# Kernel optimization log

Measured on AMD Instinct MI355X. Metric: run time of the kernel, lower is better.

Reference implementation:

```python
import jax, jax.numpy as jnp
import numpy as np

OUT_F, IN_F = 4096, 11008
NUMEL = OUT_F * IN_F            # divisible by 256
NUM_SUPER = NUMEL // 256        # super-blocks of 8 sub-blocks x 32 values


def setup_inputs() -> dict:
    key = jax.random.key(0)
    k = jax.random.split(key, 7)
    x = jax.random.normal(k[0], (64, IN_F), dtype=jnp.float32)
    packed = jax.random.randint(k[1], (NUMEL // 2,), 0, 256, dtype=jnp.int32)
    d = jax.random.uniform(k[2], (NUM_SUPER,), dtype=jnp.float32) * 0.02
    dmin = jax.random.uniform(k[3], (NUM_SUPER,), dtype=jnp.float32) * 0.02
    scales = jax.random.randint(k[4], (NUM_SUPER * 8,), 0, 64, dtype=jnp.int32)
    mins = jax.random.randint(k[5], (NUM_SUPER * 8,), 0, 64, dtype=jnp.int32)
    bias = jax.random.normal(k[6], (OUT_F,), dtype=jnp.float32) * 0.02
    return {"x": x, "packed": packed, "d": d, "dmin": dmin,
            "scales": scales, "mins": mins, "bias": bias}


def _dequant_q4k(packed, d, dmin, scales, mins):
    # unpack two 4-bit quants per byte, interleaved low/high (stack dim=1 + flatten)
    low = packed & 15
    high = (packed >> 4) & 15
    q = jnp.stack([low, high], axis=1).reshape(NUM_SUPER, 8, 32).astype(jnp.float32)
    sc = (scales.astype(jnp.float32) / 63.0).reshape(NUM_SUPER, 8, 1)
    mn = (mins.astype(jnp.float32) / 63.0).reshape(NUM_SUPER, 8, 1)
    normalized = q / 15.0 * sc + mn
    w = normalized * d.reshape(NUM_SUPER, 1, 1) + dmin.reshape(NUM_SUPER, 1, 1)
    return w.reshape(OUT_F, IN_F)


def reference(x, packed, d, dmin, scales, mins, bias):
    w = _dequant_q4k(packed, d, dmin, scales, mins)   # [OUT_F, IN_F] fp32
    return x @ w.T + bias                              # F.linear
```

## Files before the change

kernel.cpp:

```cpp
#include <hip/hip_runtime.h>
#include <stdint.h>

#define OUT_F   4096
#define IN_F    11008
#define BATCH   64
#define NSUP    43
#define SB_ROW  344
#define IPR     5504
#define NKS     12
#define XP_BYTES   (4 * 344 * 64 * 16)
#define PART_ELEMS ((size_t)NKS * BATCH * OUT_F)
#define WS_FULL    (XP_BYTES + PART_ELEMS * 4)

typedef __attribute__((ext_vector_type(8))) short  short8;
typedef __attribute__((ext_vector_type(4))) float  floatx4;
typedef __attribute__((ext_vector_type(4))) int    intx4;

__device__ __forceinline__ unsigned pack_bf16(float f0, float f1) {
    return __builtin_amdgcn_perm(__float_as_uint(f1), __float_as_uint(f0), 0x07060302u);
}

__global__ __launch_bounds__(256) void xprep_kernel(const float* __restrict__ x,
                                                    intx4* __restrict__ xp) {
    const int ksb = blockIdx.x;
    const int mt  = threadIdx.x >> 6;
    const int l   = threadIdx.x & 63;
    const int lo  = l & 15, hi = l >> 4;
    const float* src = x + (mt * 16 + lo) * IN_F + ksb * 32 + hi * 8;
    floatx4 a0 = *(const floatx4*)src;
    floatx4 a1 = *(const floatx4*)(src + 4);
    intx4 r;
    r.x = pack_bf16(a0.x, a0.y);
    r.y = pack_bf16(a0.z, a0.w);
    r.z = pack_bf16(a1.x, a1.y);
    r.w = pack_bf16(a1.z, a1.w);
    xp[(mt * 344 + ksb) * 64 + l] = r;
}

__global__ __launch_bounds__(256) void init_out_kernel(const float* __restrict__ bias,
                                                       float* __restrict__ out) {
    int i = blockIdx.x * 256 + threadIdx.x;
    out[i] = bias[i & (OUT_F - 1)];
}

__global__ __launch_bounds__(256) void reduce_kernel(const float* __restrict__ part,
                                                     const float* __restrict__ bias,
                                                     float* __restrict__ out) {
    const int i = blockIdx.x * 256 + threadIdx.x;
    float s = bias[i & (OUT_F - 1)];
    #pragma unroll
    for (int k = 0; k < NKS; ++k) s += part[(size_t)k * (BATCH * OUT_F) + i];
    out[i] = s;
}

template<bool USE_PART>
__global__ __launch_bounds__(256, 3) void qlin_main(
    const intx4* __restrict__ xp,
    const int*   __restrict__ packed,
    const float* __restrict__ dd,
    const float* __restrict__ dmn_g,
    const int*   __restrict__ scales,
    const int*   __restrict__ mins,
    float*       __restrict__ part,
    float*       __restrict__ out)
{
    __shared__ intx4 xfs[2048];
    __shared__ int   scs[512];
    __shared__ int   mns[512];
    __shared__ float dsx[64];
    __shared__ float dmx[64];

    const int nb  = blockIdx.x & 63;
    const int ks  = blockIdx.x >> 6;
    const int tid = threadIdx.x;
    const int w   = tid >> 6;
    const int l   = tid & 63;
    const int lo  = l & 15, hi = l >> 4;

    const int o    = nb * 64 + w * 16 + lo;
    const int r    = w * 16 + lo;
    const int sup0 = ks < 7 ? 4 * ks : 28 + 3 * (ks - 7);
    const int nsup = ks < 7 ? 4 : 3;

    floatx4 acc[4];
    #pragma unroll
    for (int mt = 0; mt < 4; ++mt) acc[mt] = (floatx4)0.0f;

    const int* bp0 = packed + o * IPR + sup0 * 128 + hi * 4;
    const int tr = tid & 63;
    const int og = nb * 64 + tr;

    #pragma unroll 1
    for (int s = 0; s < nsup; ++s) {
        const int sup = sup0 + s;

        intx4 br[8];
        #pragma unroll
        for (int st = 0; st < 8; ++st)
            br[st] = __builtin_nontemporal_load((const intx4*)(bp0 + s * 128 + st * 16));

        intx4 xtmp[8];
        const intx4* xsrc = xp + sup * 512;
        #pragma unroll
        for (int i = 0; i < 8; ++i) {
            const int idx = i * 256 + tid;
            xtmp[i] = xsrc[(idx >> 9) * 22016 + (idx & 511)];
        }
        intx4 sct0, sct1;
        float dtmp = 0.0f;
        if (w == 0) {
            sct0 = *(const intx4*)(scales + og * SB_ROW + sup * 8);
            sct1 = *(const intx4*)(scales + og * SB_ROW + sup * 8 + 4);
        } else if (w == 1) {
            sct0 = *(const intx4*)(mins + og * SB_ROW + sup * 8);
            sct1 = *(const intx4*)(mins + og * SB_ROW + sup * 8 + 4);
        } else if (w == 2) {
            dtmp = dd[og * NSUP + sup];
        } else {
            dtmp = dmn_g[og * NSUP + sup];
        }

        if (s > 0) __syncthreads();
        #pragma unroll
        for (int i = 0; i < 8; ++i)
            xfs[i * 256 + tid] = xtmp[i];
        if (w == 0) {
            *(intx4*)&scs[tr * 8]     = sct0;
            *(intx4*)&scs[tr * 8 + 4] = sct1;
        } else if (w == 1) {
            *(intx4*)&mns[tr * 8]     = sct0;
            *(intx4*)&mns[tr * 8 + 4] = sct1;
        } else if (w == 2) {
            dsx[tr] = dtmp;
        } else {
            dmx[tr] = dtmp;
        }
        __syncthreads();

        const float dv   = dsx[r];
        const float dmv  = dmx[r];
        const float A945 = dv * (1.0f / 945.0f);
        const float A63  = dv * (1.0f / 63.0f);
        const intx4 s0 = *(const intx4*)&scs[r * 8];
        const intx4 s1 = *(const intx4*)&scs[r * 8 + 4];
        const intx4 m0 = *(const intx4*)&mns[r * 8];
        const intx4 m1 = *(const intx4*)&mns[r * 8 + 4];

        #pragma unroll
        for (int st = 0; st < 8; ++st) {
            const int scv = (st < 4) ? s0[st & 3] : s1[st & 3];
            const int mnv = (st < 4) ? m0[st & 3] : m1[st & 3];
            const float A = A945 * (float)scv;
            const float B = fmaf(A63, (float)mnv, dmv);
            const int v0 = br[st].x, v1 = br[st].y, v2 = br[st].z, v3 = br[st].w;
            union { intx4 i; short8 s8; } uw;
            uw.i.x = pack_bf16(fmaf((float)(v0 & 15), A, B), fmaf((float)(v0 >> 4), A, B));
            uw.i.y = pack_bf16(fmaf((float)(v1 & 15), A, B), fmaf((float)(v1 >> 4), A, B));
            uw.i.z = pack_bf16(fmaf((float)(v2 & 15), A, B), fmaf((float)(v2 >> 4), A, B));
            uw.i.w = pack_bf16(fmaf((float)(v3 & 15), A, B), fmaf((float)(v3 >> 4), A, B));

            union { intx4 i; short8 s8; } u0, u1, u2, u3;
            u0.i = xfs[0 * 512 + st * 64 + l];
            u1.i = xfs[1 * 512 + st * 64 + l];
            u2.i = xfs[2 * 512 + st * 64 + l];
            u3.i = xfs[3 * 512 + st * 64 + l];
            acc[0] = __builtin_amdgcn_mfma_f32_16x16x32_bf16(u0.s8, uw.s8, acc[0], 0, 0, 0);
            acc[1] = __builtin_amdgcn_mfma_f32_16x16x32_bf16(u1.s8, uw.s8, acc[1], 0, 0, 0);
            acc[2] = __builtin_amdgcn_mfma_f32_16x16x32_bf16(u2.s8, uw.s8, acc[2], 0, 0, 0);
            acc[3] = __builtin_amdgcn_mfma_f32_16x16x32_bf16(u3.s8, uw.s8, acc[3], 0, 0, 0);
        }
    }

    if (USE_PART) {
        float* pbase = part + (size_t)ks * (BATCH * OUT_F) + o;
        #pragma unroll
        for (int mt = 0; mt < 4; ++mt) {
            #pragma unroll
            for (int rr = 0; rr < 4; ++rr)
                pbase[(mt * 16 + hi * 4 + rr) * OUT_F] = acc[mt][rr];
        }
    } else {
        #pragma unroll
        for (int mt = 0; mt < 4; ++mt) {
            #pragma unroll
            for (int rr = 0; rr < 4; ++rr)
                atomicAdd(out + (mt * 16 + hi * 4 + rr) * OUT_F + o, acc[mt][rr]);
        }
    }
}

extern "C" void kernel_launch(void* const* d_in, const int* in_sizes, int n_in,
                              void* d_out, int out_size, void* d_ws, size_t ws_size,
                              hipStream_t stream) {
    (void)in_sizes; (void)n_in; (void)out_size;
    const float* x      = (const float*)d_in[0];
    const int*   packed = (const int*)d_in[1];
    const float* d      = (const float*)d_in[2];
    const float* dmin   = (const float*)d_in[3];
    const int*   scales = (const int*)d_in[4];
    const int*   mins   = (const int*)d_in[5];
    const float* bias   = (const float*)d_in[6];
    float* out = (float*)d_out;

    const bool has_part = ws_size >= (size_t)WS_FULL;
    intx4* xp   = (intx4*)d_ws;
    float* part = (float*)((char*)d_ws + XP_BYTES);

    xprep_kernel<<<344, 256, 0, stream>>>(x, xp);

    if (has_part) {
        qlin_main<true><<<64 * NKS, 256, 0, stream>>>(
            xp, packed, d, dmin, scales, mins, part, out);
        reduce_kernel<<<(BATCH * OUT_F) / 256, 256, 0, stream>>>(part, bias, out);
    } else {
        init_out_kernel<<<(BATCH * OUT_F) / 256, 256, 0, stream>>>(bias, out);
        qlin_main<false><<<64 * NKS, 256, 0, stream>>>(
            xp, packed, d, dmin, scales, mins, part, out);
    }
}
```

Measured before the change: 166.3 us.

## Prefetch next weight block in registers and stage x via direct global-to-LDS loads

Restructures the main loop into a software pipeline. The next super-block's packed weights and scale metadata are loaded into registers while the current one is computed. Activation tiles are copied straight from global memory into LDS with global_load_lds instead of round-tripping through VGPRs. Each thread now loads its own row's scales, mins and d values directly, which removes the shared-memory staging for them. The cost is higher register pressure from double-buffered weights under a launch bound of 3 waves, plus a full vmcnt(0) wait that also drains the prefetch loads before each barrier.

```diff
diff --git a/kernel.cpp b/kernel.cpp
--- a/kernel.cpp
+++ b/kernel.cpp
@@ -16,8 +16,22 @@
 typedef __attribute__((ext_vector_type(4))) float  floatx4;
 typedef __attribute__((ext_vector_type(4))) int    intx4;
 
+template<int N> struct IC { static constexpr int value = N; };
+
 __device__ __forceinline__ unsigned pack_bf16(float f0, float f1) {
     return __builtin_amdgcn_perm(__float_as_uint(f1), __float_as_uint(f0), 0x07060302u);
+}
+
+__device__ __forceinline__ void glds16(const void* g, void* s) {
+    __builtin_amdgcn_global_load_lds(
+        (const __attribute__((address_space(1))) uint32_t*)g,
+        (__attribute__((address_space(3))) uint32_t*)s,
+        16, 0, 0);
+}
+
+__device__ __forceinline__ void wait_vm0(void) {
+    asm volatile("s_waitcnt vmcnt(0)" ::: "memory");
+    __builtin_amdgcn_sched_barrier(0);
 }
 
 __global__ __launch_bounds__(256) void xprep_kernel(const float* __restrict__ x,
@@ -65,10 +79,6 @@
     float*       __restrict__ out)
 {
     __shared__ intx4 xfs[2048];
-    __shared__ int   scs[512];
-    __shared__ int   mns[512];
-    __shared__ float dsx[64];
-    __shared__ float dmx[64];
 
     const int nb  = blockIdx.x & 63;
     const int ks  = blockIdx.x >> 6;
@@ -76,9 +86,9 @@
     const int w   = tid >> 6;
     const int l   = tid & 63;
     const int lo  = l & 15, hi = l >> 4;
+    const int wq  = tid & 192;
 
     const int o    = nb * 64 + w * 16 + lo;
-    const int r    = w * 16 + lo;
     const int sup0 = ks < 7 ? 4 * ks : 28 + 3 * (ks - 7);
     const int nsup = ks < 7 ? 4 : 3;
 
@@ -86,70 +96,42 @@
     #pragma unroll
     for (int mt = 0; mt < 4; ++mt) acc[mt] = (floatx4)0.0f;
 
-    const int* bp0 = packed + o * IPR + sup0 * 128 + hi * 4;
-    const int tr = tid & 63;
-    const int og = nb * 64 + tr;
-
-    #pragma unroll 1
-    for (int s = 0; s < nsup; ++s) {
-        const int sup = sup0 + s;
-
-        intx4 br[8];
+    const int*   bp0 = packed + o * IPR + sup0 * 128 + hi * 4;
+    const int*   scp = scales + o * SB_ROW + sup0 * 8;
+    const int*   mnp = mins   + o * SB_ROW + sup0 * 8;
+    const float* dp  = dd     + o * NSUP + sup0;
+    const float* dmp = dmn_g  + o * NSUP + sup0;
+
+    auto stage_x = [&](int sup_abs) {
+        #pragma unroll
+        for (int i = 0; i < 8; ++i) {
+            const int mt = i >> 1;
+            const intx4* src = xp + sup_abs * 512 + mt * 22016 + (i & 1) * 256 + tid;
+            glds16((const void*)src, (void*)&xfs[i * 256 + wq]);
+        }
+    };
+
+    auto load_wblk = [&](int s, intx4 br[8], intx4& s0v, intx4& s1v,
+                         intx4& m0v, intx4& m1v, float& dv, float& dmv) {
         #pragma unroll
         for (int st = 0; st < 8; ++st)
             br[st] = __builtin_nontemporal_load((const intx4*)(bp0 + s * 128 + st * 16));
-
-        intx4 xtmp[8];
-        const intx4* xsrc = xp + sup * 512;
-        #pragma unroll
-        for (int i = 0; i < 8; ++i) {
-            const int idx = i * 256 + tid;
-            xtmp[i] = xsrc[(idx >> 9) * 22016 + (idx & 511)];
-        }
-        intx4 sct0, sct1;
-        float dtmp = 0.0f;
-        if (w == 0) {
-            sct0 = *(const intx4*)(scales + og * SB_ROW + sup * 8);
-            sct1 = *(const intx4*)(scales + og * SB_ROW + sup * 8 + 4);
-        } else if (w == 1) {
-            sct0 = *(const intx4*)(mins + og * SB_ROW + sup * 8);
-            sct1 = *(const intx4*)(mins + og * SB_ROW + sup * 8 + 4);
-        } else if (w == 2) {
-            dtmp = dd[og * NSUP + sup];
-        } else {
-            dtmp = dmn_g[og * NSUP + sup];
-        }
-
-        if (s > 0) __syncthreads();
-        #pragma unroll
-        for (int i = 0; i < 8; ++i)
-            xfs[i * 256 + tid] = xtmp[i];
-        if (w == 0) {
-            *(intx4*)&scs[tr * 8]     = sct0;
-            *(intx4*)&scs[tr * 8 + 4] = sct1;
-        } else if (w == 1) {
-            *(intx4*)&mns[tr * 8]     = sct0;
-            *(intx4*)&mns[tr * 8 + 4] = sct1;
-        } else if (w == 2) {
-            dsx[tr] = dtmp;
-        } else {
-            dmx[tr] = dtmp;
-        }
-        __syncthreads();
-
-        const float dv   = dsx[r];
-        const float dmv  = dmx[r];
+        s0v = *(const intx4*)(scp + s * 8);
+        s1v = *(const intx4*)(scp + s * 8 + 4);
+        m0v = *(const intx4*)(mnp + s * 8);
+        m1v = *(const intx4*)(mnp + s * 8 + 4);
+        dv  = dp[s];
+        dmv = dmp[s];
+    };
+
+    auto compute_sup = [&](const intx4 br[8], intx4 s0v, intx4 s1v,
+                           intx4 m0v, intx4 m1v, float dv, float dmv) {
         const float A945 = dv * (1.0f / 945.0f);
         const float A63  = dv * (1.0f / 63.0f);
-        const intx4 s0 = *(const intx4*)&scs[r * 8];
-        const intx4 s1 = *(const intx4*)&scs[r * 8 + 4];
-        const intx4 m0 = *(const intx4*)&mns[r * 8];
-        const intx4 m1 = *(const intx4*)&mns[r * 8 + 4];
-
         #pragma unroll
         for (int st = 0; st < 8; ++st) {
-            const int scv = (st < 4) ? s0[st & 3] : s1[st & 3];
-            const int mnv = (st < 4) ? m0[st & 3] : m1[st & 3];
+            const int scv = (st < 4) ? s0v[st & 3] : s1v[st & 3];
+            const int mnv = (st < 4) ? m0v[st & 3] : m1v[st & 3];
             const float A = A945 * (float)scv;
             const float B = fmaf(A63, (float)mnv, dmv);
             const int v0 = br[st].x, v1 = br[st].y, v2 = br[st].z, v3 = br[st].w;
@@ -169,7 +151,38 @@
             acc[2] = __builtin_amdgcn_mfma_f32_16x16x32_bf16(u2.s8, uw.s8, acc[2], 0, 0, 0);
             acc[3] = __builtin_amdgcn_mfma_f32_16x16x32_bf16(u3.s8, uw.s8, acc[3], 0, 0, 0);
         }
-    }
+    };
+
+    auto run = [&](auto nsc) {
+        constexpr int NS = decltype(nsc)::value;
+        intx4 br[8]; intx4 s0v, s1v, m0v, m1v; float dv, dmv;
+
+        load_wblk(0, br, s0v, s1v, m0v, m1v, dv, dmv);
+        stage_x(sup0);
+        wait_vm0();
+        __builtin_amdgcn_s_barrier();
+
+        #pragma unroll
+        for (int s = 0; s < NS; ++s) {
+            intx4 brN[8]; intx4 s0N, s1N, m0N, m1N; float dvN, dmvN;
+            if (s + 1 < NS)
+                load_wblk(s + 1, brN, s0N, s1N, m0N, m1N, dvN, dmvN);
+
+            compute_sup(br, s0v, s1v, m0v, m1v, dv, dmv);
+
+            if (s + 1 < NS) {
+                __builtin_amdgcn_s_barrier();
+                stage_x(sup0 + s + 1);
+                wait_vm0();
+                __builtin_amdgcn_s_barrier();
+                #pragma unroll
+                for (int i2 = 0; i2 < 8; ++i2) br[i2] = brN[i2];
+                s0v = s0N; s1v = s1N; m0v = m0N; m1v = m1N; dv = dvN; dmv = dmvN;
+            }
+        }
+    };
+    if (nsup == 4) run(IC<4>{});
+    else           run(IC<3>{});
 
     if (USE_PART) {
         float* pbase = part + (size_t)ks * (BATCH * OUT_F) + o;
```

New measurement: 168.5 us. No clear change (+1.3%).
